# Kernel optimization log

Measured on AMD Instinct MI355X. Metric: run time of the kernel, lower is better.

Reference implementation:

```python
import jax, jax.numpy as jnp
import numpy as np

B, T, C = 4, 2048, 2048
N_HEAD, N_KV = 16, 4
HD = C // N_HEAD          # 128
N_REP = N_HEAD // N_KV    # 4


def setup_inputs() -> dict:
    key = jax.random.key(0)
    k1, k2, k3 = jax.random.split(key, 3)
    x = jax.random.normal(k1, (B, T, C), dtype=jnp.float32)
    # RoPE frequencies: complex freqs_cis stored as [T, HD//2, 2] = (cos, sin)
    inv_freq = 1.0 / (10000.0 ** (jnp.arange(0, HD, 2, dtype=jnp.float32) / HD))  # [HD//2]
    angles = jnp.arange(T, dtype=jnp.float32)[:, None] * inv_freq[None, :]        # [T, HD//2]
    freqs_cis = jnp.stack([jnp.cos(angles), jnp.sin(angles)], axis=-1)            # [T, HD//2, 2]
    w_qkv = jax.random.normal(k2, (C, (N_HEAD + 2 * N_KV) * HD), dtype=jnp.float32) * 0.02
    w_proj = jax.random.normal(k3, (C, C), dtype=jnp.float32) * 0.02
    return {"x": x, "freqs_cis": freqs_cis, "w_qkv": w_qkv, "w_proj": w_proj}


def _apply_rope(t, freqs_cis):
    # t: [B, T, H, HD]; pairs (even, odd) along last dim form complex numbers
    shp = t.shape
    t2 = t.astype(jnp.float32).reshape(*shp[:-1], HD // 2, 2)
    cos = freqs_cis[None, :, None, :, 0]  # [1, T, 1, HD//2]
    sin = freqs_cis[None, :, None, :, 1]
    re = t2[..., 0] * cos - t2[..., 1] * sin
    im = t2[..., 0] * sin + t2[..., 1] * cos
    return jnp.stack([re, im], axis=-1).reshape(shp).astype(t.dtype)


def reference(x, freqs_cis, w_qkv, w_proj):
    Bs, Ts, Cs = x.shape
    qkv = x @ w_qkv  # [B, T, (H+2KV)*HD]
    q, k, v = jnp.split(qkv, [N_HEAD * HD, N_HEAD * HD + N_KV * HD], axis=-1)
    q = q.reshape(Bs, Ts, N_HEAD, HD)
    k = k.reshape(Bs, Ts, N_KV, HD)
    v = v.reshape(Bs, Ts, N_KV, HD)
    q = _apply_rope(q, freqs_cis)
    k = _apply_rope(k, freqs_cis)
    # GQA attention without materializing repeated k/v: group query heads per kv head
    qg = q.reshape(Bs, Ts, N_KV, N_REP, HD)
    scale = 1.0 / jnp.sqrt(jnp.asarray(HD, dtype=jnp.float32))
    scores = jnp.einsum('btkrd,bskd->bkrts', qg, k) * scale  # [B, KV, REP, T, T]
    att = jax.nn.softmax(scores.astype(jnp.float32), axis=-1).astype(q.dtype)
    y = jnp.einsum('bkrts,bskd->btkrd', att, v).reshape(Bs, Ts, Cs)
    return y @ w_proj
```

## Files before the change

kernel.cpp:

```cpp
#include <hip/hip_runtime.h>

using u16 = unsigned short;
using u32 = unsigned int;
typedef float f32x4 __attribute__((ext_vector_type(4)));
typedef float f32x16 __attribute__((ext_vector_type(16)));
typedef short s16x8 __attribute__((ext_vector_type(8)));
typedef unsigned int u32x4 __attribute__((ext_vector_type(4)));

__device__ __forceinline__ u16 f2bf(float x) {
  u32 u = __float_as_uint(x);
  u += 0x7fffu + ((u >> 16) & 1u);
  return (u16)(u >> 16);
}
__device__ __forceinline__ u32 pack2bf(float lo, float hi) {
  return (u32)f2bf(lo) | ((u32)f2bf(hi) << 16);
}
__device__ __forceinline__ float bf2f(u16 v) {
  return __uint_as_float(((u32)v) << 16);
}
__device__ __forceinline__ u32 cvtpk(float lo, float hi) {
  u32 r;
  asm("v_cvt_pk_bf16_f32 %0, %1, %2" : "=v"(r) : "v"(lo), "v"(hi));
  return r;
}
__device__ __forceinline__ void plswap(u32& a, u32& b) {
  asm volatile("v_permlane32_swap_b32 %0, %1" : "+v"(a), "+v"(b));
}
__device__ __forceinline__ void gload16(const u16* g, u16* l) {
  __builtin_amdgcn_global_load_lds(
      (__attribute__((address_space(1))) void*)(u16*)g,
      (__attribute__((address_space(3))) void*)l, 16, 0, 0);
}
__device__ __forceinline__ f32x4 fzero4() {
  f32x4 v = {0.f, 0.f, 0.f, 0.f};
  return v;
}
__device__ __forceinline__ f32x16 fzero16() {
  f32x16 v = {0, 0, 0, 0, 0, 0, 0, 0, 0, 0, 0, 0, 0, 0, 0, 0};
  return v;
}
__device__ __forceinline__ void barrier_hard() {
  __builtin_amdgcn_sched_barrier(0);
  __builtin_amdgcn_s_barrier();
  __builtin_amdgcn_sched_barrier(0);
}

__global__ __launch_bounds__(256) void k_prep(const float* __restrict__ x,
                                              u16* __restrict__ xbf,
                                              const float* __restrict__ wqkv,
                                              u16* __restrict__ wqkvT,
                                              const float* __restrict__ wproj,
                                              u16* __restrict__ wprojT) {
  int bid = blockIdx.x, tid = threadIdx.x;
  if (bid < 8192) {
    int i = bid * 256 + tid;
    const float4* p = (const float4*)x;
    float4 a = p[2 * i], b = p[2 * i + 1];
    uint4 o;
    o.x = pack2bf(a.x, a.y);
    o.y = pack2bf(a.z, a.w);
    o.z = pack2bf(b.x, b.y);
    o.w = pack2bf(b.z, b.w);
    ((uint4*)xbf)[i] = o;
    return;
  }
  __shared__ float tile[64][65];
  int N, K, n0, k0;
  const float* w;
  u16* wt;
  if (bid < 9728) {
    int t = bid - 8192;
    n0 = (t % 48) * 64;
    k0 = (t / 48) * 64;
    w = wqkv; wt = wqkvT; N = 3072; K = 2048;
  } else {
    int t = bid - 9728;
    n0 = (t % 32) * 64;
    k0 = (t / 32) * 64;
    w = wproj; wt = wprojT; N = 2048; K = 2048;
  }
  int rr = tid >> 6, cc = tid & 63;
#pragma unroll
  for (int p = 0; p < 16; ++p)
    tile[p * 4 + rr][cc] = w[(size_t)(k0 + p * 4 + rr) * N + n0 + cc];
  __syncthreads();
#pragma unroll
  for (int p = 0; p < 16; ++p)
    wt[(size_t)(n0 + p * 4 + rr) * K + k0 + cc] = f2bf(tile[cc][p * 4 + rr]);
}

template <bool OBF>
__global__ __launch_bounds__(512, 2) void k_gemm8(const u16* __restrict__ A,
                                                  const u16* __restrict__ Bt,
                                                  void* __restrict__ Out, int Nd, int Kd) {
  __shared__ u16 Al[2][2][8192];
  __shared__ u16 Bl[2][2][8192];
  u32 bid = blockIdx.x, nwg = gridDim.x;
  u32 wgid = (bid & 7) * (nwg >> 3) + (bid >> 3);
  int ntn = Nd >> 8;
  int bm = wgid / ntn, bn = wgid % ntn;
  int tid = threadIdx.x, w = tid >> 6, lane = tid & 63;
  int wm = w >> 2, wn = w & 3;
  int lq = lane & 15, lg = lane >> 4;

  const u16* Ab = A + (size_t)(bm * 256) * Kd;
  const u16* Bb = Bt + (size_t)(bn * 256) * Kd;

  u32 offA[2][2], offB[2][2];
#pragma unroll
  for (int set = 0; set < 2; ++set)
#pragma unroll
    for (int inst = 0; inst < 2; ++inst) {
      int c = inst * 512 + tid;
      int ldsrow = c >> 4, sl = c & 15;
      int orig = sl ^ (ldsrow & 15);
      int pr = ldsrow * 2 + (orig >> 3);
      int kch = orig & 7;
      int rA = (pr & 63) + ((pr >> 6) & 1) * 128 + set * 64;
      int rB = (pr & 31) + (pr >> 5) * 64 + set * 32;
      offA[set][inst] = (u32)(rA * Kd + kch * 8);
      offB[set][inst] = (u32)(rB * Kd + kch * 8);
    }

  int aoff[4][2], boff[4][2];
#pragma unroll
  for (int mf = 0; mf < 4; ++mf)
#pragma unroll
    for (int kk = 0; kk < 2; ++kk) {
      int pr = wm * 64 + mf * 16 + lq;
      int slot = (((pr & 1) << 3) + kk * 4 + lg) ^ ((pr >> 1) & 15);
      aoff[mf][kk] = (pr >> 1) * 128 + slot * 8;
    }
#pragma unroll
  for (int nf = 0; nf < 4; ++nf)
#pragma unroll
    for (int kk = 0; kk < 2; ++kk) {
      int pr = wn * 32 + (nf & 1) * 16 + lq;
      int slot = (((pr & 1) << 3) + kk * 4 + lg) ^ ((pr >> 1) & 15);
      boff[nf][kk] = (pr >> 1) * 128 + slot * 8;
    }

  int ldsbase = w * 512;

  auto stgA = [&](int dbuf, int set, int u) {
    const u16* s = Ab + u * 64;
    gload16(s + offA[set][0], &Al[dbuf][set][ldsbase]);
    gload16(s + offA[set][1], &Al[dbuf][set][4096 + ldsbase]);
  };
  auto stgB = [&](int dbuf, int set, int u) {
    const u16* s = Bb + u * 64;
    gload16(s + offB[set][0], &Bl[dbuf][set][ldsbase]);
    gload16(s + offB[set][1], &Bl[dbuf][set][4096 + ldsbase]);
  };

  f32x4 acc[8][4];
#pragma unroll
  for (int m = 0; m < 8; ++m)
#pragma unroll
    for (int n = 0; n < 4; ++n) acc[m][n] = fzero4();

  s16x8 af[4][2], bf[4][2];

  auto LDA = [&](int dbuf, int set) {
#pragma unroll
    for (int mf = 0; mf < 4; ++mf)
#pragma unroll
      for (int kk = 0; kk < 2; ++kk)
        af[mf][kk] = *(const s16x8*)&Al[dbuf][set][aoff[mf][kk]];
  };
  auto LDB = [&](int dbuf, int nf0) {
#pragma unroll
    for (int nf = 0; nf < 2; ++nf)
#pragma unroll
      for (int kk = 0; kk < 2; ++kk)
        bf[nf0 + nf][kk] = *(const s16x8*)&Bl[dbuf][nf0 >> 1][boff[nf0 + nf][kk]];
  };
  auto DO_MFMA = [&](int mb, int nb) {
    __builtin_amdgcn_s_setprio(1);
#pragma unroll
    for (int mf = 0; mf < 4; ++mf)
#pragma unroll
      for (int nf = 0; nf < 2; ++nf)
#pragma unroll
        for (int kk = 0; kk < 2; ++kk)
          acc[mb + mf][nb + nf] = __builtin_amdgcn_mfma_f32_16x16x32_bf16(
              af[mf][kk], bf[nb + nf][kk], acc[mb + mf][nb + nf], 0, 0, 0);
    __builtin_amdgcn_s_setprio(0);
  };
  auto LGKM0 = [&]() {
    asm volatile("s_waitcnt lgkmcnt(0)" ::: "memory");
    __builtin_amdgcn_sched_barrier(0);
  };

  int nt = Kd >> 6;
  stgA(0, 0, 0); stgB(0, 0, 0); stgA(0, 1, 0); stgB(0, 1, 0);
  stgA(1, 0, 1); stgB(1, 1, 1); stgA(1, 1, 1);
  asm volatile("s_waitcnt vmcnt(6)" ::: "memory");
  barrier_hard();

  for (int u = 0; u < nt; ++u) {
    int c = u & 1, nc = c ^ 1;
    bool g1 = (u + 1 < nt), g2 = (u + 2 < nt);
    LDA(c, 0);
    LDB(c, 0);
    if (g1) stgB(nc, 0, u + 1);
    barrier_hard();
    LGKM0();
    DO_MFMA(0, 0);
    barrier_hard();
    LDB(c, 2);
    if (g2) stgA(c, 0, u + 2);
    barrier_hard();
    LGKM0();
    DO_MFMA(0, 2);
    barrier_hard();
    LDA(c, 1);
    if (g2) stgB(c, 1, u + 2);
    barrier_hard();
    LGKM0();
    DO_MFMA(4, 2);
    barrier_hard();
    if (g2) stgA(c, 1, u + 2);
    barrier_hard();
    DO_MFMA(4, 0);
    if (g2) {
      asm volatile("s_waitcnt vmcnt(6)" ::: "memory");
    } else {
      asm volatile("s_waitcnt vmcnt(0)" ::: "memory");
    }
    barrier_hard();
  }

  int r0 = bm * 256 + wm * 128, c0 = bn * 256 + wn * 64;
  if (OBF) {
    u16* O = (u16*)Out;
#pragma unroll
    for (int mf = 0; mf < 8; ++mf)
#pragma unroll
      for (int nf = 0; nf < 4; ++nf)
#pragma unroll
        for (int r = 0; r < 4; ++r)
          O[(size_t)(r0 + mf * 16 + lg * 4 + r) * Nd + c0 + nf * 16 + lq] =
              f2bf(acc[mf][nf][r]);
  } else {
    float* O = (float*)Out;
#pragma unroll
    for (int mf = 0; mf < 8; ++mf)
#pragma unroll
      for (int nf = 0; nf < 4; ++nf)
#pragma unroll
        for (int r = 0; r < 4; ++r)
          O[(size_t)(r0 + mf * 16 + lg * 4 + r) * Nd + c0 + nf * 16 + lq] =
              acc[mf][nf][r];
  }
}

__device__ __forceinline__ u32 rope_pair(short a, short b, float c, float s, float sc) {
  float x0 = bf2f((u16)a), x1 = bf2f((u16)b);
  return pack2bf((x0 * c - x1 * s) * sc, (x0 * s + x1 * c) * sc);
}

__global__ __launch_bounds__(256) void k_rope_all(const u16* __restrict__ qkv,
                                                  const float* __restrict__ fr,
                                                  u16* __restrict__ Q, u16* __restrict__ K,
                                                  u16* __restrict__ Vt) {
  int bid = blockIdx.x, tid = threadIdx.x;
  if (bid < 10240) {
    int idx = bid * 256 + tid;
    int row = idx / 320, g = idx % 320;
    int b = row >> 11, t = row & 2047;
    int col = g * 8;
    const u16* src = qkv + (size_t)row * 3072 + col;
    int isq = col < 2048;
    float sc = isq ? 0.127517432f : 1.0f;
    int c2 = isq ? col : col - 2048;
    int h = c2 >> 7, d = c2 & 127;
    u16* dst = isq ? (Q + ((size_t)(b * 16 + h) * 2048 + t) * 128 + d)
                   : (K + ((size_t)(b * 4 + h) * 2048 + t) * 128 + d);
    const float4* fp = (const float4*)(fr + (size_t)t * 128 + d);
    float4 f01 = fp[0], f23 = fp[1];
    s16x8 v = *(const s16x8*)src;
    uint4 o;
    o.x = rope_pair(v[0], v[1], f01.x, f01.y, sc);
    o.y = rope_pair(v[2], v[3], f01.z, f01.w, sc);
    o.z = rope_pair(v[4], v[5], f23.x, f23.y, sc);
    o.w = rope_pair(v[6], v[7], f23.z, f23.w, sc);
    *(uint4*)dst = o;
    return;
  }
  __shared__ u16 tile[128][68];
  int vb = bid - 10240;
  int t0 = (vb & 31) * 64, bh = vb >> 5;
  int b = bh >> 2, h = bh & 3;
  const u16* src = qkv + ((size_t)(b * 2048 + t0)) * 3072 + 2560 + h * 128;
#pragma unroll
  for (int i = 0; i < 4; ++i) {
    int c = tid + 256 * i;
    int r = c >> 4, col = c & 15;
    uint4 v = *(const uint4*)(src + (size_t)r * 3072 + col * 8);
    u16 e[8];
    *(uint4*)e = v;
#pragma unroll
    for (int j = 0; j < 8; ++j) tile[col * 8 + j][r] = e[j];
  }
  __syncthreads();
  u16* dst = Vt + ((size_t)bh * 128) * 2048 + t0;
#pragma unroll
  for (int i = 0; i < 4; ++i) {
    int c = tid + 256 * i;
    int d = c >> 3, part = c & 7;
    uint2 lo = *(const uint2*)&tile[d][part * 8];
    uint2 hi2 = *(const uint2*)&tile[d][part * 8 + 4];
    uint4 o = make_uint4(lo.x, lo.y, hi2.x, hi2.y);
    *(uint4*)&dst[(size_t)d * 2048 + part * 8] = o;
  }
}

__global__ __launch_bounds__(256, 2) void k_attn(const u16* __restrict__ Qg,
                                                 const u16* __restrict__ Kg,
                                                 const u16* __restrict__ Vg,
                                                 u16* __restrict__ Yg) {
  __shared__ u16 Kl[2][64 * 128];
  __shared__ u16 Vl[2][64 * 128];
  u32 bid = blockIdx.x;
  u32 wgid = (bid & 7) * 128 + (bid >> 3);
  int qt = wgid & 15, bh = wgid >> 4;
  int b = bh >> 4, h = bh & 15, kvh = h >> 2;
  int tid = threadIdx.x, w = tid >> 6, lane = tid & 63;
  int l31 = lane & 31, hi = lane >> 5;
  const u16* Qb = Qg + ((size_t)bh * 2048 + qt * 128 + w * 32 + l31) * 128;
  const u16* Kb = Kg + (size_t)(b * 4 + kvh) * 2048 * 128;
  const u16* Vb = Vg + (size_t)(b * 4 + kvh) * 128 * 2048;

  s16x8 qf[8];
#pragma unroll
  for (int kc = 0; kc < 8; ++kc)
    qf[kc] = *(const s16x8*)(Qb + kc * 16 + hi * 8);

  f32x16 o[4];
#pragma unroll
  for (int i = 0; i < 4; ++i) o[i] = fzero16();
  float l_run = 0.f;

  int krow4 = lane >> 4;
  int kc_ = lane & 15;
  u32 offV[4];
#pragma unroll
  for (int i = 0; i < 4; ++i) {
    int c = i * 256 + tid;
    int ldsrow = c >> 4, sl = c & 15;
    int orig = sl ^ (ldsrow & 15);
    int d = ldsrow * 2 + (orig >> 3);
    int kch = orig & 7;
    offV[i] = (u32)(d * 2048 + kch * 8);
  }

  auto stageK = [&](int buf, int key0) {
#pragma unroll
    for (int i = 0; i < 4; ++i) {
      int key = w * 16 + i * 4 + krow4;
      gload16(Kb + (size_t)(key0 + key) * 128 + ((kc_ ^ (key & 15)) * 8),
              &Kl[buf][(w * 16 + i * 4) * 128]);
    }
  };
  auto stageV = [&](int buf, int key0) {
#pragma unroll
    for (int i = 0; i < 4; ++i)
      gload16(Vb + key0 + offV[i], &Vl[buf][(i * 256 + w * 64) * 8]);
  };

  int swz = l31 & 15;
  auto qk2 = [&](int buf, int g, f32x16& n0, f32x16& n1) {
#pragma unroll
    for (int kc = 2 * g; kc <= 2 * g + 1; ++kc) {
      int slot = (kc * 2 + hi) ^ swz;
      s16x8 a0 = *(const s16x8*)&Kl[buf][l31 * 128 + slot * 8];
      n0 = __builtin_amdgcn_mfma_f32_32x32x16_bf16(a0, qf[kc], n0, 0, 0, 0);
      s16x8 a1 = *(const s16x8*)&Kl[buf][(32 + l31) * 128 + slot * 8];
      n1 = __builtin_amdgcn_mfma_f32_32x32x16_bf16(a1, qf[kc], n1, 0, 0, 0);
    }
  };

  stageK(0, 0);
  stageV(0, 0);
  stageK(1, 64);
  __syncthreads();
  f32x16 cA0 = fzero16(), cA1 = fzero16(), cB0 = fzero16(), cB1 = fzero16();
#pragma unroll
  for (int g = 0; g < 4; ++g) qk2(0, g, cA0, cA1);
  __syncthreads();

  auto body = [&](int t, f32x16& c0, f32x16& c1, f32x16& n0, f32x16& n1) {
    bool hasN = (t + 1 < 32), hasK2 = (t + 2 < 32);
    if (hasN) stageV((t + 1) & 1, (t + 1) * 64);
    if (hasK2) stageK(t & 1, (t + 2) * 64);
    if (hasN) {
      n0 = fzero16();
      n1 = fzero16();
    }
    int kbuf = (t + 1) & 1, vbuf = t & 1;
#pragma unroll
    for (int g = 0; g < 4; ++g) {
      __builtin_amdgcn_s_setprio(1);
      if (hasN) qk2(kbuf, g, n0, n1);
      __builtin_amdgcn_s_setprio(0);
      const f32x16& sv = (g < 2) ? c0 : c1;
      int g2 = g & 1;
      float p[8];
#pragma unroll
      for (int j = 0; j < 8; ++j) p[j] = exp2f(sv[g2 * 8 + j]);
      l_run += ((p[0] + p[1]) + (p[2] + p[3])) + ((p[4] + p[5]) + (p[6] + p[7]));
      u32 x0 = cvtpk(p[0], p[1]), y0 = cvtpk(p[4], p[5]);
      u32 x1 = cvtpk(p[2], p[3]), y1 = cvtpk(p[6], p[7]);
      plswap(x0, y0);
      plswap(x1, y1);
      u32x4 tw;
      tw.x = x0; tw.y = x1; tw.z = y0; tw.w = y1;
      s16x8 pf = __builtin_bit_cast(s16x8, tw);
      __builtin_amdgcn_s_setprio(1);
#pragma unroll
      for (int df = 0; df < 4; ++df) {
        int d = df * 32 + l31;
        int slot = (((d & 1) << 3) + g * 2 + hi) ^ ((d >> 1) & 15);
        s16x8 vf = *(const s16x8*)&Vl[vbuf][(d >> 1) * 128 + slot * 8];
        o[df] = __builtin_amdgcn_mfma_f32_32x32x16_bf16(vf, pf, o[df], 0, 0, 0);
      }
      __builtin_amdgcn_s_setprio(0);
    }
    __syncthreads();
  };

  for (int t = 0; t < 32; t += 2) {
    body(t, cA0, cA1, cB0, cB1);
    body(t + 1, cB0, cB1, cA0, cA1);
  }

  l_run += __shfl_xor(l_run, 32);
  float inv = 1.0f / l_run;
  int q = qt * 128 + w * 32 + l31;
  u16* yr = Yg + ((size_t)(b * 2048) + q) * 2048 + h * 128;
#pragma unroll
  for (int df = 0; df < 4; ++df)
#pragma unroll
    for (int q4 = 0; q4 < 4; ++q4) {
      int d0 = df * 32 + q4 * 8 + hi * 4;
      uint2 vv;
      vv.x = cvtpk(o[df][q4 * 4 + 0] * inv, o[df][q4 * 4 + 1] * inv);
      vv.y = cvtpk(o[df][q4 * 4 + 2] * inv, o[df][q4 * 4 + 3] * inv);
      *(uint2*)&yr[d0] = vv;
    }
}

extern "C" void kernel_launch(void* const* d_in, const int* in_sizes, int n_in,
                              void* d_out, int out_size, void* d_ws, size_t ws_size,
                              hipStream_t stream) {
  const float* x = (const float*)d_in[0];
  const float* fr = (const float*)d_in[1];
  const float* wqkv = (const float*)d_in[2];
  const float* wproj = (const float*)d_in[3];
  char* ws = (char*)d_ws;
  u16* xbf = (u16*)(ws + 0);
  u16* wqkvT = (u16*)(ws + 33554432);
  u16* wprojT = (u16*)(ws + 46137344);
  u16* qkv = (u16*)(ws + 54525952);
  u16* Qb = (u16*)(ws + 104857600);
  u16* Kb = (u16*)(ws + 138412032);
  u16* Vtb = (u16*)(ws + 146800640);

  k_prep<<<10752, 256, 0, stream>>>(x, xbf, wqkv, wqkvT, wproj, wprojT);
  k_gemm8<true><<<32 * 12, 512, 0, stream>>>(xbf, wqkvT, qkv, 3072, 2048);
  k_rope_all<<<10752, 256, 0, stream>>>(qkv, fr, Qb, Kb, Vtb);
  k_attn<<<1024, 256, 0, stream>>>(Qb, Kb, Vtb, xbf);
  k_gemm8<false><<<32 * 8, 512, 0, stream>>>(xbf, wprojT, d_out, 2048, 2048);
}
```

Measured before the change: 395.8 us.

## Replace software-pipelined QK/PV interleave with simple sequential per-tile loop

Removes the software pipeline that computed the next tile's QK^T scores while doing softmax and PV on the current tile. Each key tile now runs QK^T, exp and pack, then PV in sequence, with K and V for the next tile prefetched together. This cuts register pressure from the double score accumulators, but loses the overlap between exp work and MFMA issue.

Measured after the change: 393.5 us. About the same (-0.6%).

```diff
diff --git a/kernel.cpp b/kernel.cpp
--- a/kernel.cpp
+++ b/kernel.cpp
@@ -369,70 +369,73 @@
       gload16(Vb + key0 + offV[i], &Vl[buf][(i * 256 + w * 64) * 8]);
   };
 
-  int swz = l31 & 15;
-  auto qk2 = [&](int buf, int g, f32x16& n0, f32x16& n1) {
-#pragma unroll
-    for (int kc = 2 * g; kc <= 2 * g + 1; ++kc) {
-      int slot = (kc * 2 + hi) ^ swz;
-      s16x8 a0 = *(const s16x8*)&Kl[buf][l31 * 128 + slot * 8];
-      n0 = __builtin_amdgcn_mfma_f32_32x32x16_bf16(a0, qf[kc], n0, 0, 0, 0);
-      s16x8 a1 = *(const s16x8*)&Kl[buf][(32 + l31) * 128 + slot * 8];
-      n1 = __builtin_amdgcn_mfma_f32_32x32x16_bf16(a1, qf[kc], n1, 0, 0, 0);
-    }
-  };
-
   stageK(0, 0);
   stageV(0, 0);
-  stageK(1, 64);
   __syncthreads();
-  f32x16 cA0 = fzero16(), cA1 = fzero16(), cB0 = fzero16(), cB1 = fzero16();
-#pragma unroll
-  for (int g = 0; g < 4; ++g) qk2(0, g, cA0, cA1);
-  __syncthreads();
-
-  auto body = [&](int t, f32x16& c0, f32x16& c1, f32x16& n0, f32x16& n1) {
-    bool hasN = (t + 1 < 32), hasK2 = (t + 2 < 32);
-    if (hasN) stageV((t + 1) & 1, (t + 1) * 64);
-    if (hasK2) stageK(t & 1, (t + 2) * 64);
-    if (hasN) {
-      n0 = fzero16();
-      n1 = fzero16();
-    }
-    int kbuf = (t + 1) & 1, vbuf = t & 1;
+
+  for (int kt = 0; kt < 32; ++kt) {
+    int cur = kt & 1;
+    if (kt < 31) {
+      stageK(cur ^ 1, (kt + 1) * 64);
+      stageV(cur ^ 1, (kt + 1) * 64);
+    }
+
+    f32x16 s0 = fzero16(), s1 = fzero16();
+    int swz = l31 & 15;
+    __builtin_amdgcn_s_setprio(1);
+#pragma unroll
+    for (int kc = 0; kc < 8; ++kc) {
+      int slot = (kc * 2 + hi) ^ swz;
+      s16x8 a0 = *(const s16x8*)&Kl[cur][l31 * 128 + slot * 8];
+      s0 = __builtin_amdgcn_mfma_f32_32x32x16_bf16(a0, qf[kc], s0, 0, 0, 0);
+      s16x8 a1 = *(const s16x8*)&Kl[cur][(32 + l31) * 128 + slot * 8];
+      s1 = __builtin_amdgcn_mfma_f32_32x32x16_bf16(a1, qf[kc], s1, 0, 0, 0);
+    }
+    __builtin_amdgcn_s_setprio(0);
+
+    u32 pw[16];
+    float ps = 0.f;
+    auto sm_half = [&](const f32x16& sv, u32* pwg) {
+#pragma unroll
+      for (int g = 0; g < 2; ++g) {
+        float p[8];
+#pragma unroll
+        for (int j = 0; j < 8; ++j) p[j] = exp2f(sv[g * 8 + j]);
+        ps += ((p[0] + p[1]) + (p[2] + p[3])) + ((p[4] + p[5]) + (p[6] + p[7]));
+        u32 x0 = cvtpk(p[0], p[1]), y0 = cvtpk(p[4], p[5]);
+        u32 x1 = cvtpk(p[2], p[3]), y1 = cvtpk(p[6], p[7]);
+        plswap(x0, y0);
+        plswap(x1, y1);
+        pwg[g * 4 + 0] = x0;
+        pwg[g * 4 + 1] = x1;
+        pwg[g * 4 + 2] = y0;
+        pwg[g * 4 + 3] = y1;
+      }
+    };
+    sm_half(s0, pw);
+    sm_half(s1, pw + 8);
+    l_run += ps;
+
+    __builtin_amdgcn_s_setprio(1);
 #pragma unroll
     for (int g = 0; g < 4; ++g) {
-      __builtin_amdgcn_s_setprio(1);
-      if (hasN) qk2(kbuf, g, n0, n1);
-      __builtin_amdgcn_s_setprio(0);
-      const f32x16& sv = (g < 2) ? c0 : c1;
-      int g2 = g & 1;
-      float p[8];
-#pragma unroll
-      for (int j = 0; j < 8; ++j) p[j] = exp2f(sv[g2 * 8 + j]);
-      l_run += ((p[0] + p[1]) + (p[2] + p[3])) + ((p[4] + p[5]) + (p[6] + p[7]));
-      u32 x0 = cvtpk(p[0], p[1]), y0 = cvtpk(p[4], p[5]);
-      u32 x1 = cvtpk(p[2], p[3]), y1 = cvtpk(p[6], p[7]);
-      plswap(x0, y0);
-      plswap(x1, y1);
-      u32x4 tw;
-      tw.x = x0; tw.y = x1; tw.z = y0; tw.w = y1;
-      s16x8 pf = __builtin_bit_cast(s16x8, tw);
-      __builtin_amdgcn_s_setprio(1);
+      u32x4 t;
+      t.x = pw[g * 4 + 0];
+      t.y = pw[g * 4 + 1];
+      t.z = pw[g * 4 + 2];
+      t.w = pw[g * 4 + 3];
+      s16x8 pf = __builtin_bit_cast(s16x8, t);
 #pragma unroll
       for (int df = 0; df < 4; ++df) {
         int d = df * 32 + l31;
         int slot = (((d & 1) << 3) + g * 2 + hi) ^ ((d >> 1) & 15);
-        s16x8 vf = *(const s16x8*)&Vl[vbuf][(d >> 1) * 128 + slot * 8];
+        s16x8 vf = *(const s16x8*)&Vl[cur][(d >> 1) * 128 + slot * 8];
         o[df] = __builtin_amdgcn_mfma_f32_32x32x16_bf16(vf, pf, o[df], 0, 0, 0);
       }
-      __builtin_amdgcn_s_setprio(0);
-    }
+    }
+    __builtin_amdgcn_s_setprio(0);
+
     __syncthreads();
-  };
-
-  for (int t = 0; t < 32; t += 2) {
-    body(t, cA0, cA1, cB0, cB1);
-    body(t + 1, cB0, cB1, cA0, cA1);
   }
 
   l_run += __shfl_xor(l_run, 32);
```
